# Kernel tuning notes

Measured on AMD Instinct MI355X. Metric: run time of the kernel, lower is better.

## Reference

```python
import jax, jax.numpy as jnp
import numpy as np

HIDDEN_DIM = 2048
NUM_EXPERTS = 64
TOP_K = 2
NUM_TOKENS = 16384


def setup_inputs() -> dict:
    key = jax.random.key(0)
    kx, kw, kb = jax.random.split(key, 3)
    X = jax.random.normal(kx, (NUM_TOKENS, HIDDEN_DIM), dtype=jnp.float32)
    # nn.Linear(hidden_dim, num_experts): weight [num_experts, hidden_dim], bias [num_experts]
    bound = 1.0 / np.sqrt(HIDDEN_DIM)
    W = jax.random.uniform(kw, (NUM_EXPERTS, HIDDEN_DIM), minval=-bound, maxval=bound, dtype=jnp.float32)
    b = jax.random.uniform(kb, (NUM_EXPERTS,), minval=-bound, maxval=bound, dtype=jnp.float32)
    return {"X": X, "W": W, "b": b}


def reference(X, W, b):
    # router_logits = gate(X): [T, E]
    router_logits = jnp.einsum("th,eh->te", X, W) + b
    # softmax in float32 (matches dtype=torch.float)
    routing_probs = jax.nn.softmax(router_logits.astype(jnp.float32), axis=-1)
    # top-k over experts: [T, K]
    router_weights, selected_experts = jax.lax.top_k(routing_probs, TOP_K)
    # renormalize over selected experts (sum cast to X.dtype, result stays fp32 math)
    denom = jnp.sum(router_weights, axis=-1, keepdims=True).astype(X.dtype)
    router_weights = router_weights / denom
    # one-hot expert mask: [T, K, E], int64 like F.one_hot
    expert_mask = jax.nn.one_hot(selected_experts, NUM_EXPERTS, dtype=jnp.int32)
    return (router_logits, router_weights, selected_experts, expert_mask)
```

## Files before the change

### kernel.cpp

```cpp
#include <hip/hip_runtime.h>
#include <math.h>

constexpr int T_TOK = 16384;
constexpr int HDIM  = 2048;
constexpr int NEXP  = 64;
constexpr int TPB   = 32;
constexpr int MT    = TPB / 16;
constexpr int NWAVE = 8;
constexpr int KPW   = HDIM / NWAVE;
constexpr int KSTEP = 32;
constexpr int NKS   = KPW / KSTEP;

typedef __attribute__((ext_vector_type(8))) short v8s;
typedef __attribute__((ext_vector_type(4))) float v4f;

#define MFMA_BF16 __builtin_amdgcn_mfma_f32_16x16x32_bf16

static __device__ __forceinline__ void split3(float x, unsigned short& h,
                                              unsigned short& m, unsigned short& l)
{
    unsigned u0 = __float_as_uint(x);
    h = (unsigned short)(u0 >> 16);
    float r1 = x - __uint_as_float(u0 & 0xFFFF0000u);
    unsigned u1 = __float_as_uint(r1);
    m = (unsigned short)(u1 >> 16);
    float r2 = r1 - __uint_as_float(u1 & 0xFFFF0000u);
    l = (unsigned short)(__float_as_uint(r2) >> 16);
}

static __device__ __forceinline__ void frag3(const float4& x0, const float4& x1,
                                             v8s& h, v8s& m, v8s& l)
{
    unsigned short sh, sm, sl;
    split3(x0.x, sh, sm, sl); h[0]=(short)sh; m[0]=(short)sm; l[0]=(short)sl;
    split3(x0.y, sh, sm, sl); h[1]=(short)sh; m[1]=(short)sm; l[1]=(short)sl;
    split3(x0.z, sh, sm, sl); h[2]=(short)sh; m[2]=(short)sm; l[2]=(short)sl;
    split3(x0.w, sh, sm, sl); h[3]=(short)sh; m[3]=(short)sm; l[3]=(short)sl;
    split3(x1.x, sh, sm, sl); h[4]=(short)sh; m[4]=(short)sm; l[4]=(short)sl;
    split3(x1.y, sh, sm, sl); h[5]=(short)sh; m[5]=(short)sm; l[5]=(short)sl;
    split3(x1.z, sh, sm, sl); h[6]=(short)sh; m[6]=(short)sm; l[6]=(short)sl;
    split3(x1.w, sh, sm, sl); h[7]=(short)sh; m[7]=(short)sm; l[7]=(short)sl;
}

static __device__ __forceinline__ int swz_e(int tok, int e) {
    return e ^ (((tok >> 2) & 1) << 4);
}

__global__ __launch_bounds__(256)
void split_w_kernel(const float* __restrict__ W,
                    short* __restrict__ Wh,
                    short* __restrict__ Wm,
                    short* __restrict__ Wl)
{
    const int idx = blockIdx.x * 256 + threadIdx.x;
    const float* p = W + (size_t)idx * 8;
    float4 x0 = *(const float4*)p;
    float4 x1 = *(const float4*)(p + 4);
    v8s h, m, l;
    frag3(x0, x1, h, m, l);
    *(v8s*)(Wh + (size_t)idx * 8) = h;
    *(v8s*)(Wm + (size_t)idx * 8) = m;
    *(v8s*)(Wl + (size_t)idx * 8) = l;
}

__global__ __launch_bounds__(512, 4)
void moe_router_mfma(const float* __restrict__ X,
                     const short* __restrict__ Wh,
                     const short* __restrict__ Wm,
                     const short* __restrict__ Wl,
                     const float* __restrict__ Bg,
                     float* __restrict__ out)
{
    __shared__ float red[4][TPB][NEXP];

    const int tid  = threadIdx.x;
    const int lane = tid & 63;
    const int wv   = tid >> 6;
    const int r16  = lane & 15;
    const int q    = lane >> 4;
    const int tok0 = blockIdx.x * TPB;

    const float* pA = X + (size_t)(tok0 + r16) * HDIM + wv * KPW + q * 8;
    const int ob = r16 * HDIM + wv * KPW + q * 8;

    v4f acc[MT][4];
#pragma unroll
    for (int mt = 0; mt < MT; ++mt)
#pragma unroll
        for (int nt = 0; nt < 4; ++nt)
            acc[mt][nt] = (v4f){0.f, 0.f, 0.f, 0.f};

    float4 a0[MT], a1[MT];
#pragma unroll
    for (int mt = 0; mt < MT; ++mt) {
        const float* p = pA + (size_t)mt * 16 * HDIM;
        a0[mt] = *(const float4*)p;
        a1[mt] = *(const float4*)(p + 4);
    }

#pragma unroll
    for (int ks = 0; ks < NKS; ++ks) {
        const int ke = ob + ks * KSTEP;

        v8s Bh0 = *(const v8s*)(Wh + ke);
        v8s Bm0 = *(const v8s*)(Wm + ke);
        v8s Bl0 = *(const v8s*)(Wl + ke);
        v8s Bh1 = *(const v8s*)(Wh + 32768 + ke);
        v8s Bm1 = *(const v8s*)(Wm + 32768 + ke);
        v8s Bl1 = *(const v8s*)(Wl + 32768 + ke);

        v8s Ah[MT], Am[MT], Al[MT];
#pragma unroll
        for (int mt = 0; mt < MT; ++mt) frag3(a0[mt], a1[mt], Ah[mt], Am[mt], Al[mt]);

        if (ks < NKS - 1) {
            const int off = (ks + 1) * KSTEP;
#pragma unroll
            for (int mt = 0; mt < MT; ++mt) {
                const float* p = pA + (size_t)mt * 16 * HDIM + off;
                a0[mt] = *(const float4*)p;
                a1[mt] = *(const float4*)(p + 4);
            }
        }

#pragma unroll
        for (int mt = 0; mt < MT; ++mt) {
            v4f a = acc[mt][0];
            a = MFMA_BF16(Ah[mt], Bh0, a, 0, 0, 0);
            a = MFMA_BF16(Ah[mt], Bm0, a, 0, 0, 0);
            a = MFMA_BF16(Am[mt], Bh0, a, 0, 0, 0);
            a = MFMA_BF16(Ah[mt], Bl0, a, 0, 0, 0);
            a = MFMA_BF16(Al[mt], Bh0, a, 0, 0, 0);
            a = MFMA_BF16(Am[mt], Bm0, a, 0, 0, 0);
            acc[mt][0] = a;
            v4f b = acc[mt][1];
            b = MFMA_BF16(Ah[mt], Bh1, b, 0, 0, 0);
            b = MFMA_BF16(Ah[mt], Bm1, b, 0, 0, 0);
            b = MFMA_BF16(Am[mt], Bh1, b, 0, 0, 0);
            b = MFMA_BF16(Ah[mt], Bl1, b, 0, 0, 0);
            b = MFMA_BF16(Al[mt], Bh1, b, 0, 0, 0);
            b = MFMA_BF16(Am[mt], Bm1, b, 0, 0, 0);
            acc[mt][1] = b;
        }

        v8s Bh2 = *(const v8s*)(Wh + 2 * 32768 + ke);
        v8s Bm2 = *(const v8s*)(Wm + 2 * 32768 + ke);
        v8s Bl2 = *(const v8s*)(Wl + 2 * 32768 + ke);
        v8s Bh3 = *(const v8s*)(Wh + 3 * 32768 + ke);
        v8s Bm3 = *(const v8s*)(Wm + 3 * 32768 + ke);
        v8s Bl3 = *(const v8s*)(Wl + 3 * 32768 + ke);

#pragma unroll
        for (int mt = 0; mt < MT; ++mt) {
            v4f a = acc[mt][2];
            a = MFMA_BF16(Ah[mt], Bh2, a, 0, 0, 0);
            a = MFMA_BF16(Ah[mt], Bm2, a, 0, 0, 0);
            a = MFMA_BF16(Am[mt], Bh2, a, 0, 0, 0);
            a = MFMA_BF16(Ah[mt], Bl2, a, 0, 0, 0);
            a = MFMA_BF16(Al[mt], Bh2, a, 0, 0, 0);
            a = MFMA_BF16(Am[mt], Bm2, a, 0, 0, 0);
            acc[mt][2] = a;
            v4f b = acc[mt][3];
            b = MFMA_BF16(Ah[mt], Bh3, b, 0, 0, 0);
            b = MFMA_BF16(Ah[mt], Bm3, b, 0, 0, 0);
            b = MFMA_BF16(Am[mt], Bh3, b, 0, 0, 0);
            b = MFMA_BF16(Ah[mt], Bl3, b, 0, 0, 0);
            b = MFMA_BF16(Al[mt], Bh3, b, 0, 0, 0);
            b = MFMA_BF16(Am[mt], Bm3, b, 0, 0, 0);
            acc[mt][3] = b;
        }
    }

    if (wv < 4) {
#pragma unroll
        for (int mt = 0; mt < MT; ++mt)
#pragma unroll
            for (int nt = 0; nt < 4; ++nt)
#pragma unroll
                for (int r = 0; r < 4; ++r) {
                    int tok = 16 * mt + q * 4 + r;
                    int e   = 16 * nt + r16;
                    red[wv][tok][swz_e(tok, e)] = acc[mt][nt][r];
                }
    }
    __syncthreads();
    if (wv >= 4) {
#pragma unroll
        for (int mt = 0; mt < MT; ++mt)
#pragma unroll
            for (int nt = 0; nt < 4; ++nt)
#pragma unroll
                for (int r = 0; r < 4; ++r) {
                    int tok = 16 * mt + q * 4 + r;
                    int e   = 16 * nt + r16;
                    red[wv - 4][tok][swz_e(tok, e)] += acc[mt][nt][r];
                }
    }
    __syncthreads();

    if (lane < 4) {
        const int tk = wv * 4 + lane;
        const int t  = tok0 + tk;
        const int sh = lane << 4;
        float lg[NEXP];
#pragma unroll
        for (int eo = 0; eo < NEXP; ++eo) {
            int e  = (eo + sh) & (NEXP - 1);
            int es = swz_e(tk, e);
            lg[eo] = ((red[0][tk][es] + red[1][tk][es]) +
                      (red[2][tk][es] + red[3][tk][es])) + Bg[e];
        }
        float* outL = out + (size_t)t * NEXP;
#pragma unroll
        for (int eo = 0; eo < NEXP; eo += 4) {
            int e = (eo + sh) & (NEXP - 1);
            float4 v = make_float4(lg[eo], lg[eo+1], lg[eo+2], lg[eo+3]);
            *(float4*)(outL + e) = v;
        }
        float mx = lg[0];
#pragma unroll
        for (int eo = 1; eo < NEXP; ++eo) mx = fmaxf(mx, lg[eo]);
        float S = 0.f;
#pragma unroll
        for (int eo = 0; eo < NEXP; ++eo) { lg[eo] = expf(lg[eo] - mx); S += lg[eo]; }
#pragma unroll
        for (int eo = 0; eo < NEXP; ++eo) lg[eo] = lg[eo] / S;

        float v1 = lg[0]; int i1o = 0;
        float v2 = -1.0f; int i2o = 0;
#pragma unroll
        for (int eo = 1; eo < NEXP; ++eo) {
            float rv = lg[eo];
            bool g1 = rv > v1;
            bool g2 = rv > v2;
            float nv2 = g1 ? v1 : (g2 ? rv : v2);
            int   ni2 = g1 ? i1o : (g2 ? eo : i2o);
            v2 = nv2; i2o = ni2;
            v1 = g1 ? rv : v1;
            i1o = g1 ? eo : i1o;
        }
        const int i1 = (i1o + sh) & (NEXP - 1);
        const int i2 = (i2o + sh) & (NEXP - 1);
        float den = v1 + v2;
        float w1 = v1 / den, w2 = v2 / den;

        float* outW = out + (size_t)T_TOK * NEXP;
        float* outS = outW + (size_t)T_TOK * 2;
        float* outM = outS + (size_t)T_TOK * 2;
        outW[2*t+0] = w1;        outW[2*t+1] = w2;
        outS[2*t+0] = (float)i1; outS[2*t+1] = (float)i2;

        float* mrow = outM + (size_t)t * 2 * NEXP;
#pragma unroll
        for (int e = 0; e < NEXP; e += 4) {
            float4 a = make_float4(e+0==i1?1.f:0.f, e+1==i1?1.f:0.f,
                                   e+2==i1?1.f:0.f, e+3==i1?1.f:0.f);
            *(float4*)(mrow + e) = a;
            float4 b = make_float4(e+0==i2?1.f:0.f, e+1==i2?1.f:0.f,
                                   e+2==i2?1.f:0.f, e+3==i2?1.f:0.f);
            *(float4*)(mrow + NEXP + e) = b;
        }
    }
}

extern "C" void kernel_launch(void* const* d_in, const int* in_sizes, int n_in,
                              void* d_out, int out_size, void* d_ws, size_t ws_size,
                              hipStream_t stream)
{
    const float* X = (const float*)d_in[0];
    const float* W = (const float*)d_in[1];
    const float* B = (const float*)d_in[2];
    float* out     = (float*)d_out;

    short* Wh = (short*)d_ws;
    short* Wm = Wh + NEXP * HDIM;
    short* Wl = Wm + NEXP * HDIM;

    hipLaunchKernelGGL(split_w_kernel, dim3(NEXP * HDIM / 8 / 256), dim3(256),
                       0, stream, W, Wh, Wm, Wl);
    hipLaunchKernelGGL(moe_router_mfma, dim3(T_TOK / TPB), dim3(512),
                       0, stream, X, Wh, Wm, Wl, B, out);
}
```

Before: 268.4 us.

## Stage X through swizzled LDS and pre-pack W fragments in MFMA order

```diff
diff --git a/kernel.cpp b/kernel.cpp
--- a/kernel.cpp
+++ b/kernel.cpp
@@ -47,31 +47,32 @@
 }
 
 __global__ __launch_bounds__(256)
-void split_w_kernel(const float* __restrict__ W,
-                    short* __restrict__ Wh,
-                    short* __restrict__ Wm,
-                    short* __restrict__ Wl)
-{
-    const int idx = blockIdx.x * 256 + threadIdx.x;
-    const float* p = W + (size_t)idx * 8;
-    float4 x0 = *(const float4*)p;
-    float4 x1 = *(const float4*)(p + 4);
-    v8s h, m, l;
-    frag3(x0, x1, h, m, l);
-    *(v8s*)(Wh + (size_t)idx * 8) = h;
-    *(v8s*)(Wm + (size_t)idx * 8) = m;
-    *(v8s*)(Wl + (size_t)idx * 8) = l;
+void pack_w_kernel(const float* __restrict__ W, short* __restrict__ P)
+{
+    const int tid = blockIdx.x * 256 + threadIdx.x;
+    const int l   = tid & 63;
+    int g = tid >> 6;
+    const int p  = g % 3;  g /= 3;
+    const int nt = g % 4;  g /= 4;
+    const int ks = g % 8;
+    const int wv = g / 8;
+    const int r16 = l & 15, q = l >> 4;
+    const float* src = W + (size_t)(nt * 16 + r16) * HDIM + wv * KPW + ks * KSTEP + q * 8;
+    float4 x0 = *(const float4*)src;
+    float4 x1 = *(const float4*)(src + 4);
+    v8s h, m, lo;
+    frag3(x0, x1, h, m, lo);
+    v8s outv = (p == 0) ? h : (p == 1) ? m : lo;
+    *(v8s*)(P + (size_t)tid * 8) = outv;
 }
 
 __global__ __launch_bounds__(512, 4)
 void moe_router_mfma(const float* __restrict__ X,
-                     const short* __restrict__ Wh,
-                     const short* __restrict__ Wm,
-                     const short* __restrict__ Wl,
+                     const short* __restrict__ Pw,
                      const float* __restrict__ Bg,
                      float* __restrict__ out)
 {
-    __shared__ float red[4][TPB][NEXP];
+    __shared__ float smem[16384];
 
     const int tid  = threadIdx.x;
     const int lane = tid & 63;
@@ -80,8 +81,16 @@
     const int q    = lane >> 4;
     const int tok0 = blockIdx.x * TPB;
 
-    const float* pA = X + (size_t)(tok0 + r16) * HDIM + wv * KPW + q * 8;
-    const int ob = r16 * HDIM + wv * KPW + q * 8;
+    const int wrow = (lane >> 3);
+    const int sc   = ((lane & 7) ^ wrow) * 4;
+    const int srow = wrow * 32;
+    const float* pS = X + (size_t)(tok0 + wrow) * HDIM + wv * KPW + (lane & 7) * 4;
+
+    const int xslice  = wv * 2048;
+    const int rchunk0 = ((2 * q)     ^ (r16 & 7)) * 4;
+    const int rchunk1 = ((2 * q + 1) ^ (r16 & 7)) * 4;
+
+    const short* pBw = Pw + (size_t)(wv * 8) * 12 * 512 + lane * 8;
 
     v4f acc[MT][4];
 #pragma unroll
@@ -90,38 +99,46 @@
         for (int nt = 0; nt < 4; ++nt)
             acc[mt][nt] = (v4f){0.f, 0.f, 0.f, 0.f};
 
-    float4 a0[MT], a1[MT];
-#pragma unroll
-    for (int mt = 0; mt < MT; ++mt) {
-        const float* p = pA + (size_t)mt * 16 * HDIM;
-        a0[mt] = *(const float4*)p;
-        a1[mt] = *(const float4*)(p + 4);
-    }
-
-#pragma unroll
+    {
+        float4 g0 = *(const float4*)(pS + 0 * 8 * HDIM);
+        float4 g1 = *(const float4*)(pS + 1 * 8 * HDIM);
+        float4 g2 = *(const float4*)(pS + 2 * 8 * HDIM);
+        float4 g3 = *(const float4*)(pS + 3 * 8 * HDIM);
+        *(float4*)&smem[xslice + 0 * 256 + srow + sc] = g0;
+        *(float4*)&smem[xslice + 1 * 256 + srow + sc] = g1;
+        *(float4*)&smem[xslice + 2 * 256 + srow + sc] = g2;
+        *(float4*)&smem[xslice + 3 * 256 + srow + sc] = g3;
+    }
+
     for (int ks = 0; ks < NKS; ++ks) {
-        const int ke = ob + ks * KSTEP;
-
-        v8s Bh0 = *(const v8s*)(Wh + ke);
-        v8s Bm0 = *(const v8s*)(Wm + ke);
-        v8s Bl0 = *(const v8s*)(Wl + ke);
-        v8s Bh1 = *(const v8s*)(Wh + 32768 + ke);
-        v8s Bm1 = *(const v8s*)(Wm + 32768 + ke);
-        v8s Bl1 = *(const v8s*)(Wl + 32768 + ke);
+        const int cur = (ks & 1) * 1024;
+        const int nxt = ((ks + 1) & 1) * 1024;
+        const short* pBk = pBw + ks * 6144;
+
+        float4 g0, g1, g2, g3;
+        if (ks < NKS - 1) {
+            const float* pSn = pS + (ks + 1) * KSTEP;
+            g0 = *(const float4*)(pSn + 0 * 8 * HDIM);
+            g1 = *(const float4*)(pSn + 1 * 8 * HDIM);
+            g2 = *(const float4*)(pSn + 2 * 8 * HDIM);
+            g3 = *(const float4*)(pSn + 3 * 8 * HDIM);
+        }
 
         v8s Ah[MT], Am[MT], Al[MT];
 #pragma unroll
-        for (int mt = 0; mt < MT; ++mt) frag3(a0[mt], a1[mt], Ah[mt], Am[mt], Al[mt]);
-
-        if (ks < NKS - 1) {
-            const int off = (ks + 1) * KSTEP;
-#pragma unroll
-            for (int mt = 0; mt < MT; ++mt) {
-                const float* p = pA + (size_t)mt * 16 * HDIM + off;
-                a0[mt] = *(const float4*)p;
-                a1[mt] = *(const float4*)(p + 4);
-            }
-        }
+        for (int mt = 0; mt < MT; ++mt) {
+            const int rowb = xslice + cur + (16 * mt + r16) * 32;
+            float4 a0 = *(const float4*)&smem[rowb + rchunk0];
+            float4 a1 = *(const float4*)&smem[rowb + rchunk1];
+            frag3(a0, a1, Ah[mt], Am[mt], Al[mt]);
+        }
+
+        v8s Bh0 = *(const v8s*)(pBk + 0 * 512);
+        v8s Bm0 = *(const v8s*)(pBk + 1 * 512);
+        v8s Bl0 = *(const v8s*)(pBk + 2 * 512);
+        v8s Bh1 = *(const v8s*)(pBk + 3 * 512);
+        v8s Bm1 = *(const v8s*)(pBk + 4 * 512);
+        v8s Bl1 = *(const v8s*)(pBk + 5 * 512);
 
 #pragma unroll
         for (int mt = 0; mt < MT; ++mt) {
@@ -143,12 +160,19 @@
             acc[mt][1] = b;
         }
 
-        v8s Bh2 = *(const v8s*)(Wh + 2 * 32768 + ke);
-        v8s Bm2 = *(const v8s*)(Wm + 2 * 32768 + ke);
-        v8s Bl2 = *(const v8s*)(Wl + 2 * 32768 + ke);
-        v8s Bh3 = *(const v8s*)(Wh + 3 * 32768 + ke);
-        v8s Bm3 = *(const v8s*)(Wm + 3 * 32768 + ke);
-        v8s Bl3 = *(const v8s*)(Wl + 3 * 32768 + ke);
+        if (ks < NKS - 1) {
+            *(float4*)&smem[xslice + nxt + 0 * 256 + srow + sc] = g0;
+            *(float4*)&smem[xslice + nxt + 1 * 256 + srow + sc] = g1;
+            *(float4*)&smem[xslice + nxt + 2 * 256 + srow + sc] = g2;
+            *(float4*)&smem[xslice + nxt + 3 * 256 + srow + sc] = g3;
+        }
+
+        v8s Bh2 = *(const v8s*)(pBk + 6 * 512);
+        v8s Bm2 = *(const v8s*)(pBk + 7 * 512);
+        v8s Bl2 = *(const v8s*)(pBk + 8 * 512);
+        v8s Bh3 = *(const v8s*)(pBk + 9 * 512);
+        v8s Bm3 = *(const v8s*)(pBk + 10 * 512);
+        v8s Bl3 = *(const v8s*)(pBk + 11 * 512);
 
 #pragma unroll
         for (int mt = 0; mt < MT; ++mt) {
@@ -171,6 +195,9 @@
         }
     }
 
+    __syncthreads();
+    float (*red)[TPB][NEXP] = (float (*)[TPB][NEXP])smem;
+
     if (wv < 4) {
 #pragma unroll
         for (int mt = 0; mt < MT; ++mt)
@@ -272,12 +299,10 @@
     const float* B = (const float*)d_in[2];
     float* out     = (float*)d_out;
 
-    short* Wh = (short*)d_ws;
-    short* Wm = Wh + NEXP * HDIM;
-    short* Wl = Wm + NEXP * HDIM;
-
-    hipLaunchKernelGGL(split_w_kernel, dim3(NEXP * HDIM / 8 / 256), dim3(256),
-                       0, stream, W, Wh, Wm, Wl);
+    short* Pw = (short*)d_ws;
+
+    hipLaunchKernelGGL(pack_w_kernel, dim3(49152 / 256), dim3(256),
+                       0, stream, W, Pw);
     hipLaunchKernelGGL(moe_router_mfma, dim3(T_TOK / TPB), dim3(512),
-                       0, stream, X, Wh, Wm, Wl, B, out);
-}
+                       0, stream, X, Pw, B, out);
+}
```

Result: faster. 246.4 us (-8.2%).
